# Kernel optimization log

Hardware: AMD Instinct MI355X
Metric: run time of the kernel (lower is better)

Reference implementation:

```python
import jax, jax.numpy as jnp
import numpy as np

NEG = -100000.0

def setup_inputs() -> dict:
    key = jax.random.key(0)
    k1, k2 = jax.random.split(key)
    B, La, Lb, D = 64, 512, 512, 768
    a = jax.random.normal(k1, (B, La, D), dtype=jnp.float32)
    b = jax.random.normal(k2, (B, Lb, D), dtype=jnp.float32)
    mask_a = jnp.ones((B, La), dtype=jnp.int32)
    mask_b = jnp.ones((B, Lb), dtype=jnp.int32)
    return {"a": a, "mask_a": mask_a, "b": b, "mask_b": mask_b}

def reference(a, mask_a, b, mask_b):
    # e: [B, La, Lb] raw alignment scores
    e = jnp.einsum('bid,bjd->bij', a, b)
    # outer-product mask [B, La, Lb]; masked_fill where mask_e < 0.5
    mask_e = mask_a[:, :, None].astype(jnp.float32) * mask_b[:, None, :].astype(jnp.float32)
    e = jnp.where(mask_e < 0.5, NEG, e)
    # softmax over Lb -> attend b for each position of a
    t_a = jnp.einsum('bij,bjd->bid', jax.nn.softmax(e, axis=2), b)
    # softmax over La -> attend a for each position of b (transpose of attn)
    t_b = jnp.einsum('bij,bid->bjd', jax.nn.softmax(e, axis=1), a)
    m_a = jnp.concatenate((a, t_a, a - t_a, a * t_a), axis=-1)
    m_b = jnp.concatenate((b, t_b, b - t_b, b * t_b), axis=-1)
    return (m_a, m_b)
```

## Files before the change

### kernel.cpp

```cpp
#include <hip/hip_runtime.h>
#include <hip/hip_bf16.h>
#include <stdint.h>

#define B_  64
#define LA  512
#define LB  512
#define DD  768
#define NEGV -100000.0f

typedef __attribute__((ext_vector_type(8))) short bf16x8;
typedef __attribute__((ext_vector_type(4))) float f32x4;

__device__ __forceinline__ unsigned short f2bf(float x) {
    union { float f; unsigned u; } v; v.f = x;
    unsigned r = v.u + 0x7fffu + ((v.u >> 16) & 1u);
    return (unsigned short)(r >> 16);
}
__device__ __forceinline__ float bf2f(unsigned short h) {
    union { float f; unsigned u; } v; v.u = ((unsigned)h) << 16;
    return v.f;
}

template<int L, int Dm>
__global__ void conv_transpose_k(const float* __restrict__ x,
                                 unsigned short* __restrict__ xT) {
    __shared__ unsigned short tile[64][65];
    const int l0 = blockIdx.x * 64, d0 = blockIdx.y * 64, b = blockIdx.z;
    const float* xp = x + (size_t)b * L * Dm;
    unsigned short* op = xT + (size_t)b * Dm * L;
    const int c = threadIdx.x & 63, r0 = threadIdx.x >> 6;
#pragma unroll
    for (int s = 0; s < 16; ++s) {
        int r = r0 + s * 4;
        tile[r][c] = f2bf(xp[(size_t)(l0 + r) * Dm + d0 + c]);
    }
    __syncthreads();
#pragma unroll
    for (int s = 0; s < 16; ++s) {
        int r = r0 + s * 4;
        op[(size_t)(d0 + r) * L + l0 + c] = tile[c][r];
    }
}

__global__ __launch_bounds__(256, 2)
void egemm_k(const float* __restrict__ a, const float* __restrict__ b,
             const int* __restrict__ mask_a, const int* __restrict__ mask_b,
             float* __restrict__ e) {
    constexpr int BK = 32, STR = 40;
    __shared__ unsigned short Ah[128 * STR], Al[128 * STR];
    __shared__ unsigned short Bh[128 * STR], Bl[128 * STR];

    const int m0 = blockIdx.x * 128, n0 = blockIdx.y * 128, bb = blockIdx.z;
    const float* ap = a + (size_t)bb * LA * DD;
    const float* bp = b + (size_t)bb * LB * DD;
    const int tid = threadIdx.x;
    const int lane = tid & 63, w = tid >> 6;
    const int wm = (w >> 1) * 64, wn = (w & 1) * 64;
    const int lrow = lane & 15, lk = (lane >> 4) * 8;

    f32x4 acc[4][4] = {};

    const int srow = tid >> 3;
    const int scol = (tid & 7) * 4;

    for (int k0 = 0; k0 < DD; k0 += BK) {
        __syncthreads();
#pragma unroll
        for (int s = 0; s < 4; ++s) {
            int r = srow + s * 32;
            float4 va = *(const float4*)(ap + (size_t)(m0 + r) * DD + k0 + scol);
            float4 vb = *(const float4*)(bp + (size_t)(n0 + r) * DD + k0 + scol);
            ushort4 h, l;
            h.x = f2bf(va.x); l.x = f2bf(va.x - bf2f(h.x));
            h.y = f2bf(va.y); l.y = f2bf(va.y - bf2f(h.y));
            h.z = f2bf(va.z); l.z = f2bf(va.z - bf2f(h.z));
            h.w = f2bf(va.w); l.w = f2bf(va.w - bf2f(h.w));
            *(ushort4*)&Ah[r * STR + scol] = h;
            *(ushort4*)&Al[r * STR + scol] = l;
            h.x = f2bf(vb.x); l.x = f2bf(vb.x - bf2f(h.x));
            h.y = f2bf(vb.y); l.y = f2bf(vb.y - bf2f(h.y));
            h.z = f2bf(vb.z); l.z = f2bf(vb.z - bf2f(h.z));
            h.w = f2bf(vb.w); l.w = f2bf(vb.w - bf2f(h.w));
            *(ushort4*)&Bh[r * STR + scol] = h;
            *(ushort4*)&Bl[r * STR + scol] = l;
        }
        __syncthreads();

        bf16x8 ahf[4], alf[4], bhf[4], blf[4];
#pragma unroll
        for (int mi = 0; mi < 4; ++mi) {
            int r = wm + mi * 16 + lrow;
            ahf[mi] = *(const bf16x8*)&Ah[r * STR + lk];
            alf[mi] = *(const bf16x8*)&Al[r * STR + lk];
        }
#pragma unroll
        for (int ni = 0; ni < 4; ++ni) {
            int r = wn + ni * 16 + lrow;
            bhf[ni] = *(const bf16x8*)&Bh[r * STR + lk];
            blf[ni] = *(const bf16x8*)&Bl[r * STR + lk];
        }
#pragma unroll
        for (int mi = 0; mi < 4; ++mi)
#pragma unroll
            for (int ni = 0; ni < 4; ++ni) {
                acc[mi][ni] = __builtin_amdgcn_mfma_f32_16x16x32_bf16(alf[mi], bhf[ni], acc[mi][ni], 0, 0, 0);
                acc[mi][ni] = __builtin_amdgcn_mfma_f32_16x16x32_bf16(ahf[mi], blf[ni], acc[mi][ni], 0, 0, 0);
                acc[mi][ni] = __builtin_amdgcn_mfma_f32_16x16x32_bf16(ahf[mi], bhf[ni], acc[mi][ni], 0, 0, 0);
            }
    }

    const int* map = mask_a + bb * LA;
    const int* mbp = mask_b + bb * LB;
    float* ep = e + (size_t)bb * LA * LB;
    const int colbase = n0 + wn + (lane & 15);
    const int rowbase = m0 + wm + (lane >> 4) * 4;
#pragma unroll
    for (int mi = 0; mi < 4; ++mi) {
#pragma unroll
        for (int ni = 0; ni < 4; ++ni) {
            int j = colbase + ni * 16;
            float mbf = (float)mbp[j];
#pragma unroll
            for (int r = 0; r < 4; ++r) {
                int i = rowbase + mi * 16 + r;
                float mm = (float)map[i] * mbf;
                float v = (mm < 0.5f) ? NEGV : acc[mi][ni][r];
                ep[(size_t)i * LB + j] = v;
            }
        }
    }
}

__global__ void rowstats_k(const float* __restrict__ e,
                           float* __restrict__ rmax, float* __restrict__ rinv) {
    const int row = blockIdx.x * 4 + (threadIdx.x >> 6);
    const int lane = threadIdx.x & 63;
    const float* ep = e + (size_t)row * LB;
    float4 v1 = *(const float4*)(ep + lane * 8);
    float4 v2 = *(const float4*)(ep + lane * 8 + 4);
    float m = fmaxf(fmaxf(fmaxf(v1.x, v1.y), fmaxf(v1.z, v1.w)),
                    fmaxf(fmaxf(v2.x, v2.y), fmaxf(v2.z, v2.w)));
#pragma unroll
    for (int o = 32; o; o >>= 1) m = fmaxf(m, __shfl_xor(m, o));
    float s = __expf(v1.x - m) + __expf(v1.y - m) + __expf(v1.z - m) + __expf(v1.w - m)
            + __expf(v2.x - m) + __expf(v2.y - m) + __expf(v2.z - m) + __expf(v2.w - m);
#pragma unroll
    for (int o = 32; o; o >>= 1) s += __shfl_xor(s, o);
    if (lane == 0) { rmax[row] = m; rinv[row] = 1.0f / s; }
}

__global__ void colstats_k(const float* __restrict__ e,
                           float* __restrict__ cmax, float* __restrict__ cinv) {
    const int j = blockIdx.x * 256 + threadIdx.x;
    const int bb = blockIdx.y;
    const float* ep = e + (size_t)bb * LA * LB + j;
    float m0 = -3.4e38f, m1 = -3.4e38f, m2 = -3.4e38f, m3 = -3.4e38f;
    for (int i = 0; i < LA; i += 4) {
        m0 = fmaxf(m0, ep[(size_t)(i + 0) * LB]);
        m1 = fmaxf(m1, ep[(size_t)(i + 1) * LB]);
        m2 = fmaxf(m2, ep[(size_t)(i + 2) * LB]);
        m3 = fmaxf(m3, ep[(size_t)(i + 3) * LB]);
    }
    float m = fmaxf(fmaxf(m0, m1), fmaxf(m2, m3));
    float s0 = 0.f, s1 = 0.f, s2 = 0.f, s3 = 0.f;
    for (int i = 0; i < LA; i += 4) {
        s0 += __expf(ep[(size_t)(i + 0) * LB] - m);
        s1 += __expf(ep[(size_t)(i + 1) * LB] - m);
        s2 += __expf(ep[(size_t)(i + 2) * LB] - m);
        s3 += __expf(ep[(size_t)(i + 3) * LB] - m);
    }
    cmax[bb * LB + j] = m;
    cinv[bb * LB + j] = 1.0f / (s0 + s1 + s2 + s3);
}

__global__ void pgen_k(const float* __restrict__ e,
                       const float* __restrict__ rmax, const float* __restrict__ rinv,
                       const float* __restrict__ cmax, const float* __restrict__ cinv,
                       unsigned short* __restrict__ Pa, unsigned short* __restrict__ PbT) {
    __shared__ unsigned short tile[64][65];
    const int i0 = blockIdx.x * 64, j0 = blockIdx.y * 64, bb = blockIdx.z;
    const float* ep = e + (size_t)bb * LA * LB;
    const int c = threadIdx.x & 63, r0 = threadIdx.x >> 6;
    const float cm = cmax[bb * LB + j0 + c];
    const float ci = cinv[bb * LB + j0 + c];
#pragma unroll
    for (int s = 0; s < 16; ++s) {
        int r = r0 + s * 4;
        float rm = rmax[bb * LA + i0 + r];
        float ri = rinv[bb * LA + i0 + r];
        float v = ep[(size_t)(i0 + r) * LB + j0 + c];
        Pa[((size_t)bb * LA + i0 + r) * LB + j0 + c] = f2bf(__expf(v - rm) * ri);
        tile[r][c] = f2bf(__expf(v - cm) * ci);
    }
    __syncthreads();
#pragma unroll
    for (int s = 0; s < 16; ++s) {
        int r = r0 + s * 4;
        PbT[((size_t)bb * LB + j0 + r) * LA + i0 + c] = tile[c][r];
    }
}

__global__ __launch_bounds__(256, 2)
void pv_gemm_k(const unsigned short* __restrict__ P,
               const unsigned short* __restrict__ VT,
               const float* __restrict__ X,
               float* __restrict__ out) {
    constexpr int M = 512, K = 512, STR = 40;
    __shared__ unsigned short At[128 * STR], Bt[128 * STR];

    const int m0 = blockIdx.x * 128, n0 = blockIdx.y * 128, bb = blockIdx.z;
    const unsigned short* Pp = P + (size_t)bb * M * K;
    const unsigned short* Vp = VT + (size_t)bb * DD * K;
    const int tid = threadIdx.x;
    const int lane = tid & 63, w = tid >> 6;
    const int wm = (w >> 1) * 64, wn = (w & 1) * 64;
    const int lrow = lane & 15, lk = (lane >> 4) * 8;

    f32x4 acc[4][4] = {};

    for (int k0 = 0; k0 < K; k0 += 32) {
        __syncthreads();
#pragma unroll
        for (int s = 0; s < 2; ++s) {
            int ch = tid + s * 256;
            int row = ch >> 2;
            int c = (ch & 3) * 8;
            uint4 va = *(const uint4*)(Pp + (size_t)(m0 + row) * K + k0 + c);
            *(uint4*)&At[row * STR + c] = va;
            uint4 vb = *(const uint4*)(Vp + (size_t)(n0 + row) * K + k0 + c);
            *(uint4*)&Bt[row * STR + c] = vb;
        }
        __syncthreads();

        bf16x8 af[4], bf[4];
#pragma unroll
        for (int mi = 0; mi < 4; ++mi)
            af[mi] = *(const bf16x8*)&At[(wm + mi * 16 + lrow) * STR + lk];
#pragma unroll
        for (int ni = 0; ni < 4; ++ni)
            bf[ni] = *(const bf16x8*)&Bt[(wn + ni * 16 + lrow) * STR + lk];
#pragma unroll
        for (int mi = 0; mi < 4; ++mi)
#pragma unroll
            for (int ni = 0; ni < 4; ++ni)
                acc[mi][ni] = __builtin_amdgcn_mfma_f32_16x16x32_bf16(af[mi], bf[ni], acc[mi][ni], 0, 0, 0);
    }

    const float* Xp = X + (size_t)bb * M * DD;
    float* op = out + (size_t)bb * M * (4 * DD);
    const int colbase = n0 + wn + (lane & 15);
    const int rowbase = m0 + wm + (lane >> 4) * 4;
#pragma unroll
    for (int mi = 0; mi < 4; ++mi) {
#pragma unroll
        for (int ni = 0; ni < 4; ++ni) {
            int d = colbase + ni * 16;
#pragma unroll
            for (int r = 0; r < 4; ++r) {
                int i = rowbase + mi * 16 + r;
                float t = acc[mi][ni][r];
                float x = Xp[(size_t)i * DD + d];
                float* o = op + (size_t)i * (4 * DD) + d;
                o[0]      = x;
                o[DD]     = t;
                o[2 * DD] = x - t;
                o[3 * DD] = x * t;
            }
        }
    }
}

extern "C" void kernel_launch(void* const* d_in, const int* in_sizes, int n_in,
                              void* d_out, int out_size, void* d_ws, size_t ws_size,
                              hipStream_t stream) {
    const float* a      = (const float*)d_in[0];
    const int*   mask_a = (const int*)d_in[1];
    const float* b      = (const float*)d_in[2];
    const int*   mask_b = (const int*)d_in[3];
    float* out = (float*)d_out;

    uint8_t* w = (uint8_t*)d_ws;
    float* e            = (float*)w;          w += (size_t)B_ * LA * LB * 4;
    unsigned short* Pa  = (unsigned short*)w; w += (size_t)B_ * LA * LB * 2;
    unsigned short* PbT = (unsigned short*)w; w += (size_t)B_ * LB * LA * 2;
    unsigned short* bT  = (unsigned short*)w; w += (size_t)B_ * DD * LB * 2;
    unsigned short* aT  = (unsigned short*)w; w += (size_t)B_ * DD * LA * 2;
    float* rmax = (float*)w; w += (size_t)B_ * LA * 4;
    float* rinv = (float*)w; w += (size_t)B_ * LA * 4;
    float* cmax = (float*)w; w += (size_t)B_ * LB * 4;
    float* cinv = (float*)w; w += (size_t)B_ * LB * 4;

    conv_transpose_k<LA, DD><<<dim3(LA / 64, DD / 64, B_), 256, 0, stream>>>(a, aT);
    conv_transpose_k<LB, DD><<<dim3(LB / 64, DD / 64, B_), 256, 0, stream>>>(b, bT);
    egemm_k<<<dim3(LA / 128, LB / 128, B_), 256, 0, stream>>>(a, b, mask_a, mask_b, e);
    rowstats_k<<<B_ * LA / 4, 256, 0, stream>>>(e, rmax, rinv);
    colstats_k<<<dim3(LB / 256, B_), 256, 0, stream>>>(e, cmax, cinv);
    pgen_k<<<dim3(LA / 64, LB / 64, B_), 256, 0, stream>>>(e, rmax, rinv, cmax, cinv, Pa, PbT);
    float* out_mb = out + (size_t)B_ * LA * (4 * DD);
    pv_gemm_k<<<dim3(512 / 128, DD / 128, B_), 256, 0, stream>>>(Pa, bT, a, out);
    pv_gemm_k<<<dim3(512 / 128, DD / 128, B_), 256, 0, stream>>>(PbT, aT, b, out_mb);
}
```

Measured before the change: 1.449 ms.

## Precompute bf16 hi/lo splits with swizzled layout and use direct global-to-LDS loads

The prep kernel now writes bf16 hi/lo splits of a and b in an XOR-swizzled layout alongside the transposes. The score GEMM no longer converts fp32 on the fly and instead loads tiles with global_load_lds straight into unpadded, swizzled shared memory. The PV GEMMs get the same treatment, and both GEMMs remap the grid so blocks of the same batch run close together. Column statistics become a single-pass online softmax split across four row segments. Output and score stores become nontemporal. The trade-off is extra workspace traffic for the hi/lo arrays and reuse of the hi buffer for P.

```diff
diff --git a/kernel.cpp b/kernel.cpp
--- a/kernel.cpp
+++ b/kernel.cpp
@@ -1,5 +1,4 @@
 #include <hip/hip_runtime.h>
-#include <hip/hip_bf16.h>
 #include <stdint.h>
 
 #define B_  64
@@ -21,83 +20,104 @@
     return v.f;
 }
 
-template<int L, int Dm>
-__global__ void conv_transpose_k(const float* __restrict__ x,
-                                 unsigned short* __restrict__ xT) {
+#define GLD16(gp, lp) __builtin_amdgcn_global_load_lds( \
+    (const __attribute__((address_space(1))) void*)(gp), \
+    (__attribute__((address_space(3))) void*)(lp), 16, 0, 0)
+
+template<int L>
+__global__ void prep_k(const float* __restrict__ x,
+                       unsigned short* __restrict__ xT,
+                       unsigned short* __restrict__ xh,
+                       unsigned short* __restrict__ xl) {
     __shared__ unsigned short tile[64][65];
     const int l0 = blockIdx.x * 64, d0 = blockIdx.y * 64, b = blockIdx.z;
-    const float* xp = x + (size_t)b * L * Dm;
-    unsigned short* op = xT + (size_t)b * Dm * L;
-    const int c = threadIdx.x & 63, r0 = threadIdx.x >> 6;
+    const float* xp = x + (size_t)b * L * DD;
+    unsigned short* tp = xT + (size_t)b * DD * L;
+    unsigned short* hp = xh + (size_t)b * L * DD;
+    unsigned short* lp = xl + (size_t)b * L * DD;
+    const int c4 = (threadIdx.x & 15) * 4;
+    const int r0 = threadIdx.x >> 4;
+#pragma unroll
+    for (int s = 0; s < 4; ++s) {
+        const int r = r0 + s * 16;
+        const int l = l0 + r;
+        float4 v = *(const float4*)(xp + (size_t)l * DD + d0 + c4);
+        ushort4 h, lo;
+        h.x = f2bf(v.x); lo.x = f2bf(v.x - bf2f(h.x));
+        h.y = f2bf(v.y); lo.y = f2bf(v.y - bf2f(h.y));
+        h.z = f2bf(v.z); lo.z = f2bf(v.z - bf2f(h.z));
+        h.w = f2bf(v.w); lo.w = f2bf(v.w - bf2f(h.w));
+        tile[r][c4 + 0] = h.x; tile[r][c4 + 1] = h.y;
+        tile[r][c4 + 2] = h.z; tile[r][c4 + 3] = h.w;
+        const int qp = (((c4 >> 3) ^ (r >> 1)) & 3) << 3;
+        const int dp = d0 + (c4 & ~31) + qp + (c4 & 7);
+        *(ushort4*)&hp[(size_t)l * DD + dp] = h;
+        *(ushort4*)&lp[(size_t)l * DD + dp] = lo;
+    }
+    __syncthreads();
+    const int c = threadIdx.x & 63, rr = threadIdx.x >> 6;
 #pragma unroll
     for (int s = 0; s < 16; ++s) {
-        int r = r0 + s * 4;
-        tile[r][c] = f2bf(xp[(size_t)(l0 + r) * Dm + d0 + c]);
-    }
-    __syncthreads();
-#pragma unroll
-    for (int s = 0; s < 16; ++s) {
-        int r = r0 + s * 4;
-        op[(size_t)(d0 + r) * L + l0 + c] = tile[c][r];
+        const int r = rr + s * 4;
+        const int qp = (((c >> 3) ^ (r >> 1)) & 3) << 3;
+        const int cp = l0 + (c & ~31) + qp + (c & 7);
+        tp[(size_t)(d0 + r) * L + cp] = tile[c][r];
     }
 }
 
 __global__ __launch_bounds__(256, 2)
-void egemm_k(const float* __restrict__ a, const float* __restrict__ b,
+void egemm_k(const unsigned short* __restrict__ Ahg, const unsigned short* __restrict__ Alg,
+             const unsigned short* __restrict__ Bhg, const unsigned short* __restrict__ Blg,
              const int* __restrict__ mask_a, const int* __restrict__ mask_b,
              float* __restrict__ e) {
-    constexpr int BK = 32, STR = 40;
-    __shared__ unsigned short Ah[128 * STR], Al[128 * STR];
-    __shared__ unsigned short Bh[128 * STR], Bl[128 * STR];
-
-    const int m0 = blockIdx.x * 128, n0 = blockIdx.y * 128, bb = blockIdx.z;
-    const float* ap = a + (size_t)bb * LA * DD;
-    const float* bp = b + (size_t)bb * LB * DD;
+    __shared__ unsigned short Ah[128 * 32], Al[128 * 32], Bh[128 * 32], Bl[128 * 32];
+    const int loc = blockIdx.x, g = blockIdx.y;
+    const int t = loc >> 3;
+    const int bb = g * 8 + (loc & 7);
+    const int m0 = (t & 3) * 128, n0 = (t >> 2) * 128;
+
     const int tid = threadIdx.x;
     const int lane = tid & 63, w = tid >> 6;
     const int wm = (w >> 1) * 64, wn = (w & 1) * 64;
-    const int lrow = lane & 15, lk = (lane >> 4) * 8;
+    const int lrow = lane & 15, qsel = lane >> 4;
+    const int poff = ((qsel ^ (lrow >> 1)) & 3) << 3;
+
+    const size_t boff = (size_t)bb * 512 * DD;
+    const int sr0 = (2 * w) * 16 + (lane >> 2);
+    const int sc = (lane & 3) * 8;
+    const unsigned short* pa0 = Ahg + boff + (size_t)(m0 + sr0) * DD + sc;
+    const unsigned short* pa1 = pa0 + 16 * DD;
+    const unsigned short* pl0 = Alg + boff + (size_t)(m0 + sr0) * DD + sc;
+    const unsigned short* pl1 = pl0 + 16 * DD;
+    const unsigned short* pb0 = Bhg + boff + (size_t)(n0 + sr0) * DD + sc;
+    const unsigned short* pb1 = pb0 + 16 * DD;
+    const unsigned short* pm0 = Blg + boff + (size_t)(n0 + sr0) * DD + sc;
+    const unsigned short* pm1 = pm0 + 16 * DD;
+    unsigned short* la0 = &Ah[(2 * w) * 512]; unsigned short* la1 = la0 + 512;
+    unsigned short* ll0 = &Al[(2 * w) * 512]; unsigned short* ll1 = ll0 + 512;
+    unsigned short* lb0 = &Bh[(2 * w) * 512]; unsigned short* lb1 = lb0 + 512;
+    unsigned short* lm0 = &Bl[(2 * w) * 512]; unsigned short* lm1 = lm0 + 512;
 
     f32x4 acc[4][4] = {};
 
-    const int srow = tid >> 3;
-    const int scol = (tid & 7) * 4;
-
-    for (int k0 = 0; k0 < DD; k0 += BK) {
+    for (int k0 = 0; k0 < DD; k0 += 32) {
+        GLD16(pa0 + k0, la0); GLD16(pa1 + k0, la1);
+        GLD16(pl0 + k0, ll0); GLD16(pl1 + k0, ll1);
+        GLD16(pb0 + k0, lb0); GLD16(pb1 + k0, lb1);
+        GLD16(pm0 + k0, lm0); GLD16(pm1 + k0, lm1);
         __syncthreads();
-#pragma unroll
-        for (int s = 0; s < 4; ++s) {
-            int r = srow + s * 32;
-            float4 va = *(const float4*)(ap + (size_t)(m0 + r) * DD + k0 + scol);
-            float4 vb = *(const float4*)(bp + (size_t)(n0 + r) * DD + k0 + scol);
-            ushort4 h, l;
-            h.x = f2bf(va.x); l.x = f2bf(va.x - bf2f(h.x));
-            h.y = f2bf(va.y); l.y = f2bf(va.y - bf2f(h.y));
-            h.z = f2bf(va.z); l.z = f2bf(va.z - bf2f(h.z));
-            h.w = f2bf(va.w); l.w = f2bf(va.w - bf2f(h.w));
-            *(ushort4*)&Ah[r * STR + scol] = h;
-            *(ushort4*)&Al[r * STR + scol] = l;
-            h.x = f2bf(vb.x); l.x = f2bf(vb.x - bf2f(h.x));
-            h.y = f2bf(vb.y); l.y = f2bf(vb.y - bf2f(h.y));
-            h.z = f2bf(vb.z); l.z = f2bf(vb.z - bf2f(h.z));
-            h.w = f2bf(vb.w); l.w = f2bf(vb.w - bf2f(h.w));
-            *(ushort4*)&Bh[r * STR + scol] = h;
-            *(ushort4*)&Bl[r * STR + scol] = l;
+        bf16x8 ahf[4], alf[4], bhf[4], blf[4];
+#pragma unroll
+        for (int mi = 0; mi < 4; ++mi) {
+            const int R = wm + mi * 16 + lrow;
+            ahf[mi] = *(const bf16x8*)&Ah[R * 32 + poff];
+            alf[mi] = *(const bf16x8*)&Al[R * 32 + poff];
         }
-        __syncthreads();
-
-        bf16x8 ahf[4], alf[4], bhf[4], blf[4];
-#pragma unroll
-        for (int mi = 0; mi < 4; ++mi) {
-            int r = wm + mi * 16 + lrow;
-            ahf[mi] = *(const bf16x8*)&Ah[r * STR + lk];
-            alf[mi] = *(const bf16x8*)&Al[r * STR + lk];
-        }
 #pragma unroll
         for (int ni = 0; ni < 4; ++ni) {
-            int r = wn + ni * 16 + lrow;
-            bhf[ni] = *(const bf16x8*)&Bh[r * STR + lk];
-            blf[ni] = *(const bf16x8*)&Bl[r * STR + lk];
+            const int R = wn + ni * 16 + lrow;
+            bhf[ni] = *(const bf16x8*)&Bh[R * 32 + poff];
+            blf[ni] = *(const bf16x8*)&Bl[R * 32 + poff];
         }
 #pragma unroll
         for (int mi = 0; mi < 4; ++mi)
@@ -107,6 +127,7 @@
                 acc[mi][ni] = __builtin_amdgcn_mfma_f32_16x16x32_bf16(ahf[mi], blf[ni], acc[mi][ni], 0, 0, 0);
                 acc[mi][ni] = __builtin_amdgcn_mfma_f32_16x16x32_bf16(ahf[mi], bhf[ni], acc[mi][ni], 0, 0, 0);
             }
+        __syncthreads();
     }
 
     const int* map = mask_a + bb * LA;
@@ -115,20 +136,19 @@
     const int colbase = n0 + wn + (lane & 15);
     const int rowbase = m0 + wm + (lane >> 4) * 4;
 #pragma unroll
-    for (int mi = 0; mi < 4; ++mi) {
+    for (int mi = 0; mi < 4; ++mi)
 #pragma unroll
         for (int ni = 0; ni < 4; ++ni) {
-            int j = colbase + ni * 16;
-            float mbf = (float)mbp[j];
+            const int j = colbase + ni * 16;
+            const float mbf = (float)mbp[j];
 #pragma unroll
             for (int r = 0; r < 4; ++r) {
-                int i = rowbase + mi * 16 + r;
-                float mm = (float)map[i] * mbf;
-                float v = (mm < 0.5f) ? NEGV : acc[mi][ni][r];
-                ep[(size_t)i * LB + j] = v;
+                const int i = rowbase + mi * 16 + r;
+                const float mm = (float)map[i] * mbf;
+                const float v = (mm < 0.5f) ? NEGV : acc[mi][ni][r];
+                __builtin_nontemporal_store(v, &ep[(size_t)i * LB + j]);
             }
         }
-    }
 }
 
 __global__ void rowstats_k(const float* __restrict__ e,
@@ -151,26 +171,28 @@
 
 __global__ void colstats_k(const float* __restrict__ e,
                            float* __restrict__ cmax, float* __restrict__ cinv) {
-    const int j = blockIdx.x * 256 + threadIdx.x;
+    __shared__ float sm[4][64], ss[4][64];
+    const int j0 = blockIdx.x * 64;
     const int bb = blockIdx.y;
-    const float* ep = e + (size_t)bb * LA * LB + j;
-    float m0 = -3.4e38f, m1 = -3.4e38f, m2 = -3.4e38f, m3 = -3.4e38f;
-    for (int i = 0; i < LA; i += 4) {
-        m0 = fmaxf(m0, ep[(size_t)(i + 0) * LB]);
-        m1 = fmaxf(m1, ep[(size_t)(i + 1) * LB]);
-        m2 = fmaxf(m2, ep[(size_t)(i + 2) * LB]);
-        m3 = fmaxf(m3, ep[(size_t)(i + 3) * LB]);
-    }
-    float m = fmaxf(fmaxf(m0, m1), fmaxf(m2, m3));
-    float s0 = 0.f, s1 = 0.f, s2 = 0.f, s3 = 0.f;
-    for (int i = 0; i < LA; i += 4) {
-        s0 += __expf(ep[(size_t)(i + 0) * LB] - m);
-        s1 += __expf(ep[(size_t)(i + 1) * LB] - m);
-        s2 += __expf(ep[(size_t)(i + 2) * LB] - m);
-        s3 += __expf(ep[(size_t)(i + 3) * LB] - m);
-    }
-    cmax[bb * LB + j] = m;
-    cinv[bb * LB + j] = 1.0f / (s0 + s1 + s2 + s3);
+    const int jj = threadIdx.x & 63, seg = threadIdx.x >> 6;
+    const float* ep = e + (size_t)bb * LA * LB + (size_t)seg * 128 * LB + j0 + jj;
+    float m = -3.4e38f, s = 0.f;
+    for (int i = 0; i < 128; ++i) {
+        const float v = ep[(size_t)i * LB];
+        const float nm = fmaxf(m, v);
+        s = s * __expf(m - nm) + __expf(v - nm);
+        m = nm;
+    }
+    sm[seg][jj] = m; ss[seg][jj] = s;
+    __syncthreads();
+    if (seg == 0) {
+        const float m0 = sm[0][jj], m1 = sm[1][jj], m2 = sm[2][jj], m3 = sm[3][jj];
+        const float M = fmaxf(fmaxf(m0, m1), fmaxf(m2, m3));
+        const float S = ss[0][jj] * __expf(m0 - M) + ss[1][jj] * __expf(m1 - M)
+                      + ss[2][jj] * __expf(m2 - M) + ss[3][jj] * __expf(m3 - M);
+        cmax[bb * LB + j0 + jj] = M;
+        cinv[bb * LB + j0 + jj] = 1.0f / S;
+    }
 }
 
 __global__ void pgen_k(const float* __restrict__ e,
@@ -185,18 +207,22 @@
     const float ci = cinv[bb * LB + j0 + c];
 #pragma unroll
     for (int s = 0; s < 16; ++s) {
-        int r = r0 + s * 4;
-        float rm = rmax[bb * LA + i0 + r];
-        float ri = rinv[bb * LA + i0 + r];
-        float v = ep[(size_t)(i0 + r) * LB + j0 + c];
-        Pa[((size_t)bb * LA + i0 + r) * LB + j0 + c] = f2bf(__expf(v - rm) * ri);
+        const int r = r0 + s * 4;
+        const float rm = rmax[bb * LA + i0 + r];
+        const float ri = rinv[bb * LA + i0 + r];
+        const float v = ep[(size_t)(i0 + r) * LB + j0 + c];
+        const int qp = (((c >> 3) ^ (r >> 1)) & 3) << 3;
+        const int jp = j0 + (c & ~31) + qp + (c & 7);
+        Pa[((size_t)bb * LA + i0 + r) * LB + jp] = f2bf(__expf(v - rm) * ri);
         tile[r][c] = f2bf(__expf(v - cm) * ci);
     }
     __syncthreads();
 #pragma unroll
     for (int s = 0; s < 16; ++s) {
-        int r = r0 + s * 4;
-        PbT[((size_t)bb * LB + j0 + r) * LA + i0 + c] = tile[c][r];
+        const int r = r0 + s * 4;
+        const int qp = (((c >> 3) ^ (r >> 1)) & 3) << 3;
+        const int ip = i0 + (c & ~31) + qp + (c & 7);
+        PbT[((size_t)bb * LB + j0 + r) * LA + ip] = tile[c][r];
     }
 }
 
@@ -205,69 +231,71 @@
                const unsigned short* __restrict__ VT,
                const float* __restrict__ X,
                float* __restrict__ out) {
-    constexpr int M = 512, K = 512, STR = 40;
-    __shared__ unsigned short At[128 * STR], Bt[128 * STR];
-
-    const int m0 = blockIdx.x * 128, n0 = blockIdx.y * 128, bb = blockIdx.z;
-    const unsigned short* Pp = P + (size_t)bb * M * K;
-    const unsigned short* Vp = VT + (size_t)bb * DD * K;
+    constexpr int K = 512;
+    __shared__ unsigned short At[128 * 32], Bt[128 * 32];
+    const int loc = blockIdx.x, g = blockIdx.y;
+    const int t = loc >> 3;
+    const int bb = g * 8 + (loc & 7);
+    const int m0 = (t & 3) * 128, n0 = (t >> 2) * 128;
+
     const int tid = threadIdx.x;
     const int lane = tid & 63, w = tid >> 6;
     const int wm = (w >> 1) * 64, wn = (w & 1) * 64;
-    const int lrow = lane & 15, lk = (lane >> 4) * 8;
+    const int lrow = lane & 15, qsel = lane >> 4;
+    const int poff = ((qsel ^ (lrow >> 1)) & 3) << 3;
+
+    const unsigned short* Pp = P + (size_t)bb * 512 * K;
+    const unsigned short* Vp = VT + (size_t)bb * DD * K;
+    const int sr0 = (2 * w) * 16 + (lane >> 2);
+    const int sc = (lane & 3) * 8;
+    const unsigned short* p0 = Pp + (size_t)(m0 + sr0) * K + sc;
+    const unsigned short* p1 = p0 + 16 * K;
+    const unsigned short* v0 = Vp + (size_t)(n0 + sr0) * K + sc;
+    const unsigned short* v1 = v0 + 16 * K;
+    unsigned short* lA0 = &At[(2 * w) * 512]; unsigned short* lA1 = lA0 + 512;
+    unsigned short* lB0 = &Bt[(2 * w) * 512]; unsigned short* lB1 = lB0 + 512;
 
     f32x4 acc[4][4] = {};
-
     for (int k0 = 0; k0 < K; k0 += 32) {
+        GLD16(p0 + k0, lA0); GLD16(p1 + k0, lA1);
+        GLD16(v0 + k0, lB0); GLD16(v1 + k0, lB1);
         __syncthreads();
-#pragma unroll
-        for (int s = 0; s < 2; ++s) {
-            int ch = tid + s * 256;
-            int row = ch >> 2;
-            int c = (ch & 3) * 8;
-            uint4 va = *(const uint4*)(Pp + (size_t)(m0 + row) * K + k0 + c);
-            *(uint4*)&At[row * STR + c] = va;
-            uint4 vb = *(const uint4*)(Vp + (size_t)(n0 + row) * K + k0 + c);
-            *(uint4*)&Bt[row * STR + c] = vb;
-        }
+        bf16x8 af[4], bf_[4];
+#pragma unroll
+        for (int mi = 0; mi < 4; ++mi)
+            af[mi] = *(const bf16x8*)&At[(wm + mi * 16 + lrow) * 32 + poff];
+#pragma unroll
+        for (int ni = 0; ni < 4; ++ni)
+            bf_[ni] = *(const bf16x8*)&Bt[(wn + ni * 16 + lrow) * 32 + poff];
+#pragma unroll
+        for (int mi = 0; mi < 4; ++mi)
+#pragma unroll
+            for (int ni = 0; ni < 4; ++ni)
+                acc[mi][ni] = __builtin_amdgcn_mfma_f32_16x16x32_bf16(af[mi], bf_[ni], acc[mi][ni], 0, 0, 0);
         __syncthreads();
-
-        bf16x8 af[4], bf[4];
-#pragma unroll
-        for (int mi = 0; mi < 4; ++mi)
-            af[mi] = *(const bf16x8*)&At[(wm + mi * 16 + lrow) * STR + lk];
-#pragma unroll
-        for (int ni = 0; ni < 4; ++ni)
-            bf[ni] = *(const bf16x8*)&Bt[(wn + ni * 16 + lrow) * STR + lk];
-#pragma unroll
-        for (int mi = 0; mi < 4; ++mi)
-#pragma unroll
-            for (int ni = 0; ni < 4; ++ni)
-                acc[mi][ni] = __builtin_amdgcn_mfma_f32_16x16x32_bf16(af[mi], bf[ni], acc[mi][ni], 0, 0, 0);
-    }
-
-    const float* Xp = X + (size_t)bb * M * DD;
-    float* op = out + (size_t)bb * M * (4 * DD);
+    }
+
+    const float* Xp = X + (size_t)bb * 512 * DD;
+    float* op = out + (size_t)bb * 512 * (4 * DD);
     const int colbase = n0 + wn + (lane & 15);
     const int rowbase = m0 + wm + (lane >> 4) * 4;
 #pragma unroll
-    for (int mi = 0; mi < 4; ++mi) {
+    for (int mi = 0; mi < 4; ++mi)
 #pragma unroll
         for (int ni = 0; ni < 4; ++ni) {
-            int d = colbase + ni * 16;
+            const int d = colbase + ni * 16;
 #pragma unroll
             for (int r = 0; r < 4; ++r) {
-                int i = rowbase + mi * 16 + r;
-                float t = acc[mi][ni][r];
-                float x = Xp[(size_t)i * DD + d];
+                const int i = rowbase + mi * 16 + r;
+                const float tv = acc[mi][ni][r];
+                const float xv = Xp[(size_t)i * DD + d];
                 float* o = op + (size_t)i * (4 * DD) + d;
-                o[0]      = x;
-                o[DD]     = t;
-                o[2 * DD] = x - t;
-                o[3 * DD] = x * t;
+                __builtin_nontemporal_store(xv, o);
+                __builtin_nontemporal_store(tv, o + DD);
+                __builtin_nontemporal_store(xv - tv, o + 2 * DD);
+                __builtin_nontemporal_store(xv * tv, o + 3 * DD);
             }
         }
-    }
 }
 
 extern "C" void kernel_launch(void* const* d_in, const int* in_sizes, int n_in,
@@ -281,22 +309,26 @@
 
     uint8_t* w = (uint8_t*)d_ws;
     float* e            = (float*)w;          w += (size_t)B_ * LA * LB * 4;
-    unsigned short* Pa  = (unsigned short*)w; w += (size_t)B_ * LA * LB * 2;
-    unsigned short* PbT = (unsigned short*)w; w += (size_t)B_ * LB * LA * 2;
+    unsigned short* aT  = (unsigned short*)w; w += (size_t)B_ * DD * LA * 2;
     unsigned short* bT  = (unsigned short*)w; w += (size_t)B_ * DD * LB * 2;
-    unsigned short* aT  = (unsigned short*)w; w += (size_t)B_ * DD * LA * 2;
+    unsigned short* ahi = (unsigned short*)w; w += (size_t)B_ * LA * DD * 2;
+    unsigned short* alo = (unsigned short*)w; w += (size_t)B_ * LA * DD * 2;
+    unsigned short* bhi = (unsigned short*)w; w += (size_t)B_ * LB * DD * 2;
+    unsigned short* blo = (unsigned short*)w; w += (size_t)B_ * LB * DD * 2;
     float* rmax = (float*)w; w += (size_t)B_ * LA * 4;
     float* rinv = (float*)w; w += (size_t)B_ * LA * 4;
     float* cmax = (float*)w; w += (size_t)B_ * LB * 4;
     float* cinv = (float*)w; w += (size_t)B_ * LB * 4;
-
-    conv_transpose_k<LA, DD><<<dim3(LA / 64, DD / 64, B_), 256, 0, stream>>>(a, aT);
-    conv_transpose_k<LB, DD><<<dim3(LB / 64, DD / 64, B_), 256, 0, stream>>>(b, bT);
-    egemm_k<<<dim3(LA / 128, LB / 128, B_), 256, 0, stream>>>(a, b, mask_a, mask_b, e);
+    unsigned short* Pa  = ahi;
+    unsigned short* PbT = ahi + (size_t)B_ * LA * LB;
+
+    prep_k<LA><<<dim3(LA / 64, DD / 64, B_), 256, 0, stream>>>(a, aT, ahi, alo);
+    prep_k<LB><<<dim3(LB / 64, DD / 64, B_), 256, 0, stream>>>(b, bT, bhi, blo);
+    egemm_k<<<dim3(128, 8), 256, 0, stream>>>(ahi, alo, bhi, blo, mask_a, mask_b, e);
     rowstats_k<<<B_ * LA / 4, 256, 0, stream>>>(e, rmax, rinv);
-    colstats_k<<<dim3(LB / 256, B_), 256, 0, stream>>>(e, cmax, cinv);
+    colstats_k<<<dim3(LB / 64, B_), 256, 0, stream>>>(e, cmax, cinv);
     pgen_k<<<dim3(LA / 64, LB / 64, B_), 256, 0, stream>>>(e, rmax, rinv, cmax, cinv, Pa, PbT);
     float* out_mb = out + (size_t)B_ * LA * (4 * DD);
-    pv_gemm_k<<<dim3(512 / 128, DD / 128, B_), 256, 0, stream>>>(Pa, bT, a, out);
-    pv_gemm_k<<<dim3(512 / 128, DD / 128, B_), 256, 0, stream>>>(PbT, aT, b, out_mb);
-}
+    pv_gemm_k<<<dim3(192, 8), 256, 0, stream>>>(Pa, bT, a, out);
+    pv_gemm_k<<<dim3(192, 8), 256, 0, stream>>>(PbT, aT, b, out_mb);
+}
```

Result: faster. 1.362 ms (-6.0%).
